# Optimization experiments

Measured on AMD Instinct MI355X. Metric: run time of the kernel, lower is better.

Reference implementation:

```python
import jax, jax.numpy as jnp
import numpy as np

B, L, H, NH, V = 16, 2048, 512, 8, 32000
HH = H // NH  # 64


def setup_inputs() -> dict:
    key = jax.random.key(0)
    ks = jax.random.split(key, 12)
    rn = lambda k, shape, s=0.02: jax.random.normal(k, shape, jnp.float32) * s
    inp = {
        "seq": jax.random.randint(ks[0], (B, L), 0, V),
        # Encoder params
        "embed": rn(ks[1], (V, H)),
        "ff_w1": rn(ks[2], (H, 2 * H)), "ff_b1": jnp.zeros((2 * H,), jnp.float32),
        "ff_w2": rn(ks[3], (2 * H, H)), "ff_b2": jnp.zeros((H,), jnp.float32),
        "ln_g": jnp.ones((H,), jnp.float32), "ln_b": jnp.zeros((H,), jnp.float32),
        # per-head projections, stacked: [NH, H, HH]
        "wk": rn(ks[4], (NH, H, HH)), "bk": jnp.zeros((NH, HH), jnp.float32),
        "wv": rn(ks[5], (NH, H, HH)), "bv": jnp.zeros((NH, HH), jnp.float32),
        "wq": rn(ks[6], (NH, H, HH)), "bq": jnp.zeros((NH, HH), jnp.float32),
        # output projections
        "w_op": rn(ks[7], (H, H)), "b_op": jnp.zeros((H,), jnp.float32),
        "w_out": rn(ks[8], (H, V)), "b_out": jnp.zeros((V,), jnp.float32),
    }
    return inp


def _encoder(seq, embed, ff_w1, ff_b1, ff_w2, ff_b2, ln_g, ln_b):
    e = embed[seq]                                        # [B, L, H]
    f = jnp.maximum(e @ ff_w1 + ff_b1, 0.0) @ ff_w2 + ff_b2
    x = e + f
    mu = x.mean(-1, keepdims=True)
    var = x.var(-1, keepdims=True)
    return (x - mu) * jax.lax.rsqrt(var + 1e-5) * ln_g + ln_b


def reference(seq, embed, ff_w1, ff_b1, ff_w2, ff_b2, ln_g, ln_b,
              wk, bk, wv, bv, wq, bq, w_op, b_op, w_out, b_out):
    h_all = _encoder(seq, embed, ff_w1, ff_b1, ff_w2, ff_b2, ln_g, ln_b)  # [B,L,H]
    b = h_all.shape[0]
    hk = h_all[:, :-1]  # steps t = 0..L-2
    # precompute all per-step k/v projections, time-major for scan: [L-1, B, NH, HH]
    k_all = jnp.einsum('blh,nhd->lbnd', hk, wk) + bk
    v_all = jnp.einsum('blh,nhd->lbnd', hk, wv) + bv

    def step(M, kv):
        k, v = kv                                          # [B, NH, HH]
        vp = jnp.einsum('bnij,bnj->bni', M, k)             # M @ k
        nrm = jnp.sum(k * k, -1, keepdims=True) + 1e-6
        delta = v - vp / nrm
        M = M + delta[..., :, None] * k[..., None, :]      # rank-1 update
        return M, None

    M0 = jnp.zeros((b, NH, HH, HH), h_all.dtype)
    M, _ = jax.lax.scan(step, M0, (k_all, v_all))

    q = jnp.einsum('bh,nhd->bnd', h_all[:, -1], wq) + bq   # [B, NH, HH]
    ctx = jnp.einsum('bnij,bnj->bni', M, q).reshape(b, NH * HH)
    return (ctx @ w_op + b_op) @ w_out + b_out             # [B, V]
```

## Files before the change

### kernel.cpp

```cpp
#include <hip/hip_runtime.h>
#include <hip/hip_bf16.h>

#define B_   16
#define L_   2048
#define H_   512
#define NH_  8
#define HH_  64
#define V_   32000
#define T_   32768
#define H2_  1024
#define LM_  2047
#define SB_  32
#define NBATCH_ 64

typedef __attribute__((ext_vector_type(8))) short  short8;
typedef __attribute__((ext_vector_type(4))) float  floatx4;
typedef unsigned int u32;

__device__ inline unsigned short f2b(float x) {
  __hip_bfloat16 h = __float2bfloat16(x);
  return *reinterpret_cast<unsigned short*>(&h);
}

__device__ inline void gload_lds16(const float* g, float* l) {
  __builtin_amdgcn_global_load_lds(
      (const __attribute__((address_space(1))) u32*)g,
      (__attribute__((address_space(3))) u32*)l, 16, 0, 0);
}

template<int CTRL>
__device__ inline float dpp_add(float x) {
  union { float f; int i; } u, r;
  u.f = x;
  r.i = __builtin_amdgcn_update_dpp(u.i, u.i, CTRL, 0xF, 0xF, false);
  return x + r.f;
}

__global__ __launch_bounds__(256) void prep_kernel(
    const float* __restrict__ w1, const float* __restrict__ w2,
    const float* __restrict__ wk, const float* __restrict__ wv,
    const float* __restrict__ bk, const float* __restrict__ bv,
    unsigned short* __restrict__ W1T, unsigned short* __restrict__ W2T,
    unsigned short* __restrict__ WkvT, float* __restrict__ bkv)
{
  int id = blockIdx.x * 256 + threadIdx.x;
  { int n = id >> 9, k = id & 511;
    W1T[id] = f2b(w1[(size_t)k * H2_ + n]); }
  { int n = id >> 10, k = id & 1023;
    W2T[id] = f2b(w2[(size_t)k * H_ + n]); }
  { int j = id >> 9, h = id & 511;
    float val;
    if (j < 512) val = wk[((size_t)(j >> 6) * H_ + h) * HH_ + (j & 63)];
    else { int jj = j - 512; val = wv[((size_t)(jj >> 6) * H_ + h) * HH_ + (jj & 63)]; }
    WkvT[id] = f2b(val); }
  if (id < 1024) bkv[id] = (id < 512) ? bk[id] : bv[id - 512];
}

__global__ __launch_bounds__(256) void gather_kernel(
    const int* __restrict__ seq, const float* __restrict__ embed,
    unsigned short* __restrict__ E)
{
  int t = blockIdx.x * 4 + (threadIdx.x >> 6);
  int lane = threadIdx.x & 63;
  const float* er = embed + (size_t)seq[t] * H_;
  float4 a = *(const float4*)(er + lane * 8);
  float4 b = *(const float4*)(er + lane * 8 + 4);
  uint4 o;
  o.x = (unsigned)f2b(a.x) | ((unsigned)f2b(a.y) << 16);
  o.y = (unsigned)f2b(a.z) | ((unsigned)f2b(a.w) << 16);
  o.z = (unsigned)f2b(b.x) | ((unsigned)f2b(b.y) << 16);
  o.w = (unsigned)f2b(b.z) | ((unsigned)f2b(b.w) << 16);
  *(uint4*)(E + (size_t)t * H_ + lane * 8) = o;
}

template<int KDIM, int NDIM, int EPI>
__global__ __launch_bounds__(256) void gemm_bt(
    const unsigned short* __restrict__ A, const unsigned short* __restrict__ BT,
    const float* __restrict__ bias, void* __restrict__ outp)
{
  __shared__ uint4 smv[2048];
  char* As = (char*)smv;
  char* Bs = As + 16384;
  const int tid = threadIdx.x;
  const int t0 = blockIdx.x * 128;
  const int n0 = blockIdx.y * 128;
  const int wid = tid >> 6, lane = tid & 63;
  const int wm = wid >> 1, wn = wid & 1;
  const int lhi = lane >> 4, llo = lane & 15;

  floatx4 acc[4][4];
  #pragma unroll
  for (int m = 0; m < 4; ++m)
    #pragma unroll
    for (int n = 0; n < 4; ++n)
      acc[m][n] = (floatx4){0.f, 0.f, 0.f, 0.f};

  for (int k0 = 0; k0 < KDIM; k0 += 64) {
    #pragma unroll
    for (int i = 0; i < 4; ++i) {
      int idx = tid + i * 256;
      int row = idx >> 3, c = idx & 7;
      uint4 va = *(const uint4*)(A  + (size_t)(t0 + row) * KDIM + k0 + c * 8);
      uint4 vb = *(const uint4*)(BT + (size_t)(n0 + row) * KDIM + k0 + c * 8);
      int off = row * 128 + ((c * 16) ^ ((row & 7) << 4));
      *(uint4*)(As + off) = va;
      *(uint4*)(Bs + off) = vb;
    }
    __syncthreads();
    #pragma unroll
    for (int kk = 0; kk < 2; ++kk) {
      short8 af[4], bfr[4];
      #pragma unroll
      for (int s = 0; s < 4; ++s) {
        int arow = wm * 64 + s * 16 + llo;
        af[s]  = *(const short8*)(As + arow * 128 + ((kk * 64 + lhi * 16) ^ ((arow & 7) << 4)));
        int brow = wn * 64 + s * 16 + llo;
        bfr[s] = *(const short8*)(Bs + brow * 128 + ((kk * 64 + lhi * 16) ^ ((brow & 7) << 4)));
      }
      #pragma unroll
      for (int m = 0; m < 4; ++m)
        #pragma unroll
        for (int n = 0; n < 4; ++n)
          acc[m][n] = __builtin_amdgcn_mfma_f32_16x16x32_bf16(af[m], bfr[n], acc[m][n], 0, 0, 0);
    }
    __syncthreads();
  }

  #pragma unroll
  for (int m = 0; m < 4; ++m) {
    int grow0 = t0 + wm * 64 + m * 16 + lhi * 4;
    #pragma unroll
    for (int n = 0; n < 4; ++n) {
      int gcol = n0 + wn * 64 + n * 16 + llo;
      float bb = bias[gcol];
      #pragma unroll
      for (int r = 0; r < 4; ++r) {
        int grow = grow0 + r;
        float v = acc[m][n][r] + bb;
        if (EPI == 0) {
          v = fmaxf(v, 0.f);
          ((unsigned short*)outp)[(size_t)grow * NDIM + gcol] = f2b(v);
        } else if (EPI == 1) {
          ((float*)outp)[(size_t)grow * NDIM + gcol] = v;
        } else {
          int l = grow & (L_ - 1), b = grow >> 11;
          if (l != LM_)
            ((float*)outp)[((size_t)(l * B_ + b)) * H2_ + gcol] = v;
        }
      }
    }
  }
}

__global__ __launch_bounds__(256) void ln_kernel(
    const float* __restrict__ X, const int* __restrict__ seq,
    const float* __restrict__ embed, const float* __restrict__ gam,
    const float* __restrict__ bet, unsigned short* __restrict__ Hbf,
    float* __restrict__ Hlast)
{
  int t = blockIdx.x * 4 + (threadIdx.x >> 6);
  int lane = threadIdx.x & 63;
  const float* xr = X + (size_t)t * H_;
  const float* er = embed + (size_t)seq[t] * H_;
  float4 x0 = *(const float4*)(xr + lane * 8);
  float4 x1 = *(const float4*)(xr + lane * 8 + 4);
  float4 e0 = *(const float4*)(er + lane * 8);
  float4 e1 = *(const float4*)(er + lane * 8 + 4);
  float xs[8] = {x0.x + e0.x, x0.y + e0.y, x0.z + e0.z, x0.w + e0.w,
                 x1.x + e1.x, x1.y + e1.y, x1.z + e1.z, x1.w + e1.w};
  float sum = 0.f, sq = 0.f;
  #pragma unroll
  for (int j = 0; j < 8; ++j) { sum += xs[j]; sq = fmaf(xs[j], xs[j], sq); }
  #pragma unroll
  for (int m = 1; m < 64; m <<= 1) { sum += __shfl_xor(sum, m); sq += __shfl_xor(sq, m); }
  float mu = sum * (1.f / H_);
  float var = sq * (1.f / H_) - mu * mu;
  float rs = rsqrtf(var + 1e-5f);
  float4 g0 = *(const float4*)(gam + lane * 8);
  float4 g1 = *(const float4*)(gam + lane * 8 + 4);
  float4 b0 = *(const float4*)(bet + lane * 8);
  float4 b1 = *(const float4*)(bet + lane * 8 + 4);
  float gs[8] = {g0.x, g0.y, g0.z, g0.w, g1.x, g1.y, g1.z, g1.w};
  float bs[8] = {b0.x, b0.y, b0.z, b0.w, b1.x, b1.y, b1.z, b1.w};
  float h[8];
  #pragma unroll
  for (int j = 0; j < 8; ++j) h[j] = (xs[j] - mu) * rs * gs[j] + bs[j];
  uint4 o;
  o.x = (unsigned)f2b(h[0]) | ((unsigned)f2b(h[1]) << 16);
  o.y = (unsigned)f2b(h[2]) | ((unsigned)f2b(h[3]) << 16);
  o.z = (unsigned)f2b(h[4]) | ((unsigned)f2b(h[5]) << 16);
  o.w = (unsigned)f2b(h[6]) | ((unsigned)f2b(h[7]) << 16);
  *(uint4*)(Hbf + (size_t)t * H_ + lane * 8) = o;
  if ((t & (L_ - 1)) == LM_) {
    int bi = t >> 11;
    #pragma unroll
    for (int j = 0; j < 8; ++j) Hlast[bi * H_ + lane * 8 + j] = h[j];
  }
}

__global__ __launch_bounds__(64) void qproj_kernel(
    const float* __restrict__ Hlast, const float* __restrict__ wq,
    const float* __restrict__ bq, float* __restrict__ qbuf)
{
  int b = blockIdx.x >> 3, n = blockIdx.x & 7;
  int d = threadIdx.x;
  float acc = bq[n * 64 + d];
  const float* w = wq + (size_t)n * H_ * HH_ + d;
  const float* h = Hlast + b * H_;
  for (int k = 0; k < H_; ++k) acc = fmaf(h[k], w[(size_t)k * HH_], acc);
  qbuf[b * H_ + n * 64 + d] = acc;
}

__global__ __launch_bounds__(256) void rnk_kernel(
    const float* __restrict__ KV, float* __restrict__ rn2)
{
  int w = blockIdx.x * 4 + (threadIdx.x >> 6);
  if (w >= LM_ * B_) return;
  int lane = threadIdx.x & 63;
  int l = w >> 4, b = w & 15;
  const float* p = KV + (size_t)(l * B_ + b) * H2_ + lane * 8;
  float4 a = *(const float4*)p;
  float4 c = *(const float4*)(p + 4);
  float s = a.x*a.x + a.y*a.y + a.z*a.z + a.w*a.w
          + c.x*c.x + c.y*c.y + c.z*c.z + c.w*c.w;
  s = dpp_add<0xB1>(s); s = dpp_add<0x4E>(s); s = dpp_add<0x141>(s);
  if ((lane & 7) == 0)
    rn2[((size_t)b * 8 + (lane >> 3)) * 2048 + l] = 1.0f / (s + 1e-6f);
}

__device__ inline void dstep(float (&M)[8], const float* kvb, const float* rnrow,
                             int s, int cg, int iglob) {
  float4 ka = *(const float4*)(kvb + s * 128 + cg * 8);
  float4 kb = *(const float4*)(kvb + s * 128 + cg * 8 + 4);
  float vi = kvb[s * 128 + 64 + iglob];
  float rr = rnrow[s];
  float pa = M[0] * ka.x;
  pa = fmaf(M[1], ka.y, pa); pa = fmaf(M[2], ka.z, pa); pa = fmaf(M[3], ka.w, pa);
  float pb = M[4] * kb.x;
  pb = fmaf(M[5], kb.y, pb); pb = fmaf(M[6], kb.z, pb); pb = fmaf(M[7], kb.w, pb);
  float p = pa + pb;
  p = dpp_add<0xB1>(p); p = dpp_add<0x4E>(p); p = dpp_add<0x141>(p);
  float d = fmaf(-p, rr, vi);
  M[0] = fmaf(d, ka.x, M[0]); M[1] = fmaf(d, ka.y, M[1]);
  M[2] = fmaf(d, ka.z, M[2]); M[3] = fmaf(d, ka.w, M[3]);
  M[4] = fmaf(d, kb.x, M[4]); M[5] = fmaf(d, kb.y, M[5]);
  M[6] = fmaf(d, kb.z, M[6]); M[7] = fmaf(d, kb.w, M[7]);
}

__global__ __launch_bounds__(256) void scan_kernel(
    const float* __restrict__ KV, const float* __restrict__ rn2,
    const float* __restrict__ qbuf, float* __restrict__ ctx)
{
  __shared__ float kv[2][SB_ * 128];
  const int bid = blockIdx.x;
  const int pair = bid >> 1, half = bid & 1;
  const int b = pair >> 3, n = pair & 7;
  const int tid = threadIdx.x;
  const int w = tid >> 6, lane = tid & 63;
  const int r = lane >> 3, cg = lane & 7;
  const int iglob = half * 32 + w * 8 + r;

  const int col4 = (lane & 31) * 4;
  const int goffc = (col4 < 64) ? col4 : (col4 + 448);
  const float* gsrc = KV + (size_t)(8 * w + (lane >> 5)) * 16384
                         + (size_t)b * 1024 + n * 64 + goffc;
  const float* rnbp = rn2 + (size_t)(b * 8 + n) * 2048;

  float M[8];
  #pragma unroll
  for (int c = 0; c < 8; ++c) M[c] = 0.f;

  #pragma unroll
  for (int j = 0; j < 4; ++j)
    gload_lds16(gsrc + j * 32768, &kv[0][(4 * w + j) * 256]);
  gsrc += 524288;
  __syncthreads();

  for (int bt = 0; bt < NBATCH_; ++bt) {
    const int cur = bt & 1;
    if (bt + 1 < NBATCH_) {
      int adj = (bt + 1 == NBATCH_ - 1 && w == 3 && (lane >> 5)) ? 16384 : 0;
      gload_lds16(gsrc + 0 * 32768,       &kv[cur ^ 1][(4 * w + 0) * 256]);
      gload_lds16(gsrc + 1 * 32768,       &kv[cur ^ 1][(4 * w + 1) * 256]);
      gload_lds16(gsrc + 2 * 32768,       &kv[cur ^ 1][(4 * w + 2) * 256]);
      gload_lds16(gsrc + 3 * 32768 - adj, &kv[cur ^ 1][(4 * w + 3) * 256]);
      gsrc += 524288;
    }
    const float* kvb = &kv[cur][0];
    const float* rnrow = rnbp + bt * SB_;
    if (bt < NBATCH_ - 1) {
      #pragma unroll
      for (int s = 0; s < SB_; ++s) dstep(M, kvb, rnrow, s, cg, iglob);
    } else {
      #pragma unroll
      for (int s = 0; s < SB_ - 1; ++s) dstep(M, kvb, rnrow, s, cg, iglob);
    }
    __syncthreads();
  }

  const float* qp = qbuf + b * H_ + n * 64 + cg * 8;
  float4 qa = *(const float4*)(qp);
  float4 qb = *(const float4*)(qp + 4);
  float p = M[0] * qa.x;
  p = fmaf(M[1], qa.y, p); p = fmaf(M[2], qa.z, p); p = fmaf(M[3], qa.w, p);
  p = fmaf(M[4], qb.x, p); p = fmaf(M[5], qb.y, p);
  p = fmaf(M[6], qb.z, p); p = fmaf(M[7], qb.w, p);
  p = dpp_add<0xB1>(p); p = dpp_add<0x4E>(p); p = dpp_add<0x141>(p);
  if (cg == 0) ctx[b * H_ + n * 64 + iglob] = p;
}

__global__ __launch_bounds__(256) void opproj_kernel(
    const float* __restrict__ ctx, const float* __restrict__ wop,
    const float* __restrict__ bop, float* __restrict__ o1t)
{
  int id = blockIdx.x * 256 + threadIdx.x;
  int b = id >> 9, h = id & 511;
  float acc = bop[h];
  const float* c = ctx + b * H_;
  for (int k = 0; k < H_; ++k) acc = fmaf(c[k], wop[(size_t)k * H_ + h], acc);
  o1t[h * B_ + b] = acc;
}

__global__ __launch_bounds__(256) void outproj_kernel(
    const float* __restrict__ o1t, const float* __restrict__ wout,
    const float* __restrict__ bout, float* __restrict__ out)
{
  __shared__ float o1s[H_ * B_];
  for (int idx = threadIdx.x; idx < H_ * B_; idx += 256) o1s[idx] = o1t[idx];
  __syncthreads();
  int v = blockIdx.x * 256 + threadIdx.x;
  float bo = bout[v];
  float acc[B_];
  #pragma unroll
  for (int b = 0; b < B_; ++b) acc[b] = bo;
  for (int h = 0; h < H_; ++h) {
    float w = wout[(size_t)h * V_ + v];
    const float4* op = (const float4*)&o1s[h * B_];
    float4 a0 = op[0], a1 = op[1], a2 = op[2], a3 = op[3];
    float oa[16] = {a0.x,a0.y,a0.z,a0.w, a1.x,a1.y,a1.z,a1.w,
                    a2.x,a2.y,a2.z,a2.w, a3.x,a3.y,a3.z,a3.w};
    #pragma unroll
    for (int b = 0; b < B_; ++b) acc[b] = fmaf(oa[b], w, acc[b]);
  }
  #pragma unroll
  for (int b = 0; b < B_; ++b) out[(size_t)b * V_ + v] = acc[b];
}

extern "C" void kernel_launch(void* const* d_in, const int* in_sizes, int n_in,
                              void* d_out, int out_size, void* d_ws, size_t ws_size,
                              hipStream_t stream)
{
  const int*   seq   = (const int*)d_in[0];
  const float* embed = (const float*)d_in[1];
  const float* ffw1  = (const float*)d_in[2];
  const float* ffb1  = (const float*)d_in[3];
  const float* ffw2  = (const float*)d_in[4];
  const float* ffb2  = (const float*)d_in[5];
  const float* lng   = (const float*)d_in[6];
  const float* lnb   = (const float*)d_in[7];
  const float* wk    = (const float*)d_in[8];
  const float* bk    = (const float*)d_in[9];
  const float* wv    = (const float*)d_in[10];
  const float* bv    = (const float*)d_in[11];
  const float* wq    = (const float*)d_in[12];
  const float* bq    = (const float*)d_in[13];
  const float* wop   = (const float*)d_in[14];
  const float* bop   = (const float*)d_in[15];
  const float* wout  = (const float*)d_in[16];
  const float* bout  = (const float*)d_in[17];

  char* ws = (char*)d_ws;
  const size_t MB = 1024 * 1024;
  unsigned short* W1T   = (unsigned short*)(ws + 0 * MB);
  unsigned short* W2T   = (unsigned short*)(ws + 1 * MB);
  unsigned short* WkvT  = (unsigned short*)(ws + 2 * MB);
  float*          bkv   = (float*)(ws + 3 * MB);
  float*          Hlast = (float*)(ws + 3 * MB + 8192);
  float*          qbuf  = (float*)(ws + 3 * MB + 8192 + 32768);
  float*          ctx   = (float*)(ws + 3 * MB + 8192 + 2 * 32768);
  float*          o1t   = (float*)(ws + 3 * MB + 8192 + 3 * 32768);
  unsigned short* E     = (unsigned short*)(ws + 4 * MB);
  unsigned short* Hbf   = E;
  float*          rn2   = (float*)(ws + 4 * MB);
  unsigned short* Hmid  = (unsigned short*)(ws + 36 * MB);
  float*          X     = (float*)(ws + 100 * MB);
  float*          KV    = (float*)(ws + 36 * MB);

  prep_kernel  <<<dim3(2048), dim3(256), 0, stream>>>(ffw1, ffw2, wk, wv, bk, bv, W1T, W2T, WkvT, bkv);
  gather_kernel<<<dim3(8192), dim3(256), 0, stream>>>(seq, embed, E);
  gemm_bt<512, 1024, 0><<<dim3(256, 8), dim3(256), 0, stream>>>(E, W1T, ffb1, Hmid);
  gemm_bt<1024, 512, 1><<<dim3(256, 4), dim3(256), 0, stream>>>(Hmid, W2T, ffb2, X);
  ln_kernel    <<<dim3(8192), dim3(256), 0, stream>>>(X, seq, embed, lng, lnb, Hbf, Hlast);
  gemm_bt<512, 1024, 2><<<dim3(256, 8), dim3(256), 0, stream>>>(Hbf, WkvT, bkv, KV);
  rnk_kernel   <<<dim3(8188), dim3(256), 0, stream>>>(KV, rn2);
  qproj_kernel <<<dim3(128), dim3(64), 0, stream>>>(Hlast, wq, bq, qbuf);
  scan_kernel  <<<dim3(256), dim3(256), 0, stream>>>(KV, rn2, qbuf, ctx);
  opproj_kernel<<<dim3(32), dim3(256), 0, stream>>>(ctx, wop, bop, o1t);
  outproj_kernel<<<dim3(125), dim3(256), 0, stream>>>(o1t, wout, bout, (float*)d_out);
}
```

Measured before the change: 702.6 us.

## Replace forward matrix scan with backward vector recurrence on the query

Instead of evolving the 64x64 state matrix forward over all steps and multiplying by q at the end, the scan propagates the query vector backward through the transposed rank-1 updates, accumulating the context as a sum of value vectors weighted by projected query dot products. Each (batch, head) pair becomes a single 64-lane wave holding one vector element per lane, and a register ring prefetches k, v and the inverse norms RD steps ahead. This cuts the per-step work from a matrix-vector product plus a rank-1 update to two vector ops. The price is a full-wave reduction with a readlane on every step's serial chain, and only 128 single-wave blocks run.

```diff
diff --git a/kernel.cpp b/kernel.cpp
--- a/kernel.cpp
+++ b/kernel.cpp
@@ -10,22 +10,14 @@
 #define T_   32768
 #define H2_  1024
 #define LM_  2047
-#define SB_  32
-#define NBATCH_ 64
+#define RD_  16
 
 typedef __attribute__((ext_vector_type(8))) short  short8;
 typedef __attribute__((ext_vector_type(4))) float  floatx4;
-typedef unsigned int u32;
 
 __device__ inline unsigned short f2b(float x) {
   __hip_bfloat16 h = __float2bfloat16(x);
   return *reinterpret_cast<unsigned short*>(&h);
-}
-
-__device__ inline void gload_lds16(const float* g, float* l) {
-  __builtin_amdgcn_global_load_lds(
-      (const __attribute__((address_space(1))) u32*)g,
-      (__attribute__((address_space(3))) u32*)l, 16, 0, 0);
 }
 
 template<int CTRL>
@@ -34,6 +26,19 @@
   u.f = x;
   r.i = __builtin_amdgcn_update_dpp(u.i, u.i, CTRL, 0xF, 0xF, false);
   return x + r.f;
+}
+
+__device__ inline float wave_total(float x) {
+  x = dpp_add<0xB1>(x);
+  x = dpp_add<0x4E>(x);
+  x = dpp_add<0x141>(x);
+  x = dpp_add<0x140>(x);
+  x = dpp_add<0x142>(x);
+  x = dpp_add<0x143>(x);
+  union { float f; int i; } u;
+  u.f = x;
+  u.i = __builtin_amdgcn_readlane(u.i, 63);
+  return u.f;
 }
 
 __global__ __launch_bounds__(256) void prep_kernel(
@@ -228,85 +233,54 @@
     rn2[((size_t)b * 8 + (lane >> 3)) * 2048 + l] = 1.0f / (s + 1e-6f);
 }
 
-__device__ inline void dstep(float (&M)[8], const float* kvb, const float* rnrow,
-                             int s, int cg, int iglob) {
-  float4 ka = *(const float4*)(kvb + s * 128 + cg * 8);
-  float4 kb = *(const float4*)(kvb + s * 128 + cg * 8 + 4);
-  float vi = kvb[s * 128 + 64 + iglob];
-  float rr = rnrow[s];
-  float pa = M[0] * ka.x;
-  pa = fmaf(M[1], ka.y, pa); pa = fmaf(M[2], ka.z, pa); pa = fmaf(M[3], ka.w, pa);
-  float pb = M[4] * kb.x;
-  pb = fmaf(M[5], kb.y, pb); pb = fmaf(M[6], kb.z, pb); pb = fmaf(M[7], kb.w, pb);
-  float p = pa + pb;
-  p = dpp_add<0xB1>(p); p = dpp_add<0x4E>(p); p = dpp_add<0x141>(p);
-  float d = fmaf(-p, rr, vi);
-  M[0] = fmaf(d, ka.x, M[0]); M[1] = fmaf(d, ka.y, M[1]);
-  M[2] = fmaf(d, ka.z, M[2]); M[3] = fmaf(d, ka.w, M[3]);
-  M[4] = fmaf(d, kb.x, M[4]); M[5] = fmaf(d, kb.y, M[5]);
-  M[6] = fmaf(d, kb.z, M[6]); M[7] = fmaf(d, kb.w, M[7]);
-}
-
-__global__ __launch_bounds__(256) void scan_kernel(
+__global__ __launch_bounds__(64, 1) void scanb_kernel(
     const float* __restrict__ KV, const float* __restrict__ rn2,
     const float* __restrict__ qbuf, float* __restrict__ ctx)
 {
-  __shared__ float kv[2][SB_ * 128];
-  const int bid = blockIdx.x;
-  const int pair = bid >> 1, half = bid & 1;
+  const int pair = blockIdx.x;
+  const int lane = threadIdx.x;
   const int b = pair >> 3, n = pair & 7;
-  const int tid = threadIdx.x;
-  const int w = tid >> 6, lane = tid & 63;
-  const int r = lane >> 3, cg = lane & 7;
-  const int iglob = half * 32 + w * 8 + r;
-
-  const int col4 = (lane & 31) * 4;
-  const int goffc = (col4 < 64) ? col4 : (col4 + 448);
-  const float* gsrc = KV + (size_t)(8 * w + (lane >> 5)) * 16384
-                         + (size_t)b * 1024 + n * 64 + goffc;
-  const float* rnbp = rn2 + (size_t)(b * 8 + n) * 2048;
-
-  float M[8];
-  #pragma unroll
-  for (int c = 0; c < 8; ++c) M[c] = 0.f;
-
-  #pragma unroll
-  for (int j = 0; j < 4; ++j)
-    gload_lds16(gsrc + j * 32768, &kv[0][(4 * w + j) * 256]);
-  gsrc += 524288;
-  __syncthreads();
-
-  for (int bt = 0; bt < NBATCH_; ++bt) {
-    const int cur = bt & 1;
-    if (bt + 1 < NBATCH_) {
-      int adj = (bt + 1 == NBATCH_ - 1 && w == 3 && (lane >> 5)) ? 16384 : 0;
-      gload_lds16(gsrc + 0 * 32768,       &kv[cur ^ 1][(4 * w + 0) * 256]);
-      gload_lds16(gsrc + 1 * 32768,       &kv[cur ^ 1][(4 * w + 1) * 256]);
-      gload_lds16(gsrc + 2 * 32768,       &kv[cur ^ 1][(4 * w + 2) * 256]);
-      gload_lds16(gsrc + 3 * 32768 - adj, &kv[cur ^ 1][(4 * w + 3) * 256]);
-      gsrc += 524288;
+  const float* kbase = KV + (size_t)b * H2_ + n * 64 + lane;
+  const float* vbase = kbase + 512;
+  const float* rnp = rn2 + (size_t)pair * 2048;
+
+  float z = qbuf[pair * 64 + lane];
+  float cx = 0.f;
+
+  float kk[RD_], vv[RD_], rr[RD_];
+  #pragma unroll
+  for (int j = 0; j < RD_; ++j) {
+    int l = 2046 - j;
+    kk[j] = kbase[(size_t)l * (B_ * H2_)];
+    vv[j] = vbase[(size_t)l * (B_ * H2_)];
+    rr[j] = rnp[l];
+  }
+
+  for (int it = 0; it < 127; ++it) {
+    int tbase = 2046 - it * RD_;
+    #pragma unroll
+    for (int j = 0; j < RD_; ++j) {
+      int t = tbase - j;
+      float s = wave_total(kk[j] * z);
+      float c = s * rr[j];
+      z  = fmaf(-c, kk[j], z);
+      cx = fmaf(s,  vv[j], cx);
+      int lnx = t - RD_;
+      if (lnx < 0) lnx = 0;
+      kk[j] = kbase[(size_t)lnx * (B_ * H2_)];
+      vv[j] = vbase[(size_t)lnx * (B_ * H2_)];
+      rr[j] = rnp[lnx];
     }
-    const float* kvb = &kv[cur][0];
-    const float* rnrow = rnbp + bt * SB_;
-    if (bt < NBATCH_ - 1) {
-      #pragma unroll
-      for (int s = 0; s < SB_; ++s) dstep(M, kvb, rnrow, s, cg, iglob);
-    } else {
-      #pragma unroll
-      for (int s = 0; s < SB_ - 1; ++s) dstep(M, kvb, rnrow, s, cg, iglob);
-    }
-    __syncthreads();
-  }
-
-  const float* qp = qbuf + b * H_ + n * 64 + cg * 8;
-  float4 qa = *(const float4*)(qp);
-  float4 qb = *(const float4*)(qp + 4);
-  float p = M[0] * qa.x;
-  p = fmaf(M[1], qa.y, p); p = fmaf(M[2], qa.z, p); p = fmaf(M[3], qa.w, p);
-  p = fmaf(M[4], qb.x, p); p = fmaf(M[5], qb.y, p);
-  p = fmaf(M[6], qb.z, p); p = fmaf(M[7], qb.w, p);
-  p = dpp_add<0xB1>(p); p = dpp_add<0x4E>(p); p = dpp_add<0x141>(p);
-  if (cg == 0) ctx[b * H_ + n * 64 + iglob] = p;
+  }
+  #pragma unroll
+  for (int j = 0; j < 15; ++j) {
+    float s = wave_total(kk[j] * z);
+    float c = s * rr[j];
+    z  = fmaf(-c, kk[j], z);
+    cx = fmaf(s,  vv[j], cx);
+  }
+
+  ctx[pair * 64 + lane] = cx;
 }
 
 __global__ __launch_bounds__(256) void opproj_kernel(
@@ -394,7 +368,7 @@
   gemm_bt<512, 1024, 2><<<dim3(256, 8), dim3(256), 0, stream>>>(Hbf, WkvT, bkv, KV);
   rnk_kernel   <<<dim3(8188), dim3(256), 0, stream>>>(KV, rn2);
   qproj_kernel <<<dim3(128), dim3(64), 0, stream>>>(Hlast, wq, bq, qbuf);
-  scan_kernel  <<<dim3(256), dim3(256), 0, stream>>>(KV, rn2, qbuf, ctx);
+  scanb_kernel <<<dim3(128), dim3(64), 0, stream>>>(KV, rn2, qbuf, ctx);
   opproj_kernel<<<dim3(32), dim3(256), 0, stream>>>(ctx, wop, bop, o1t);
   outproj_kernel<<<dim3(125), dim3(256), 0, stream>>>(o1t, wout, bout, (float*)d_out);
 }
```

Result: faster. 661.0 us (-5.9%).
